# Kernel tuning notes

Hardware: AMD Instinct MI355X
Metric: run time of the kernel (lower is better)

The kernel has to match this reference:

```python
import jax, jax.numpy as jnp
import numpy as np


def _gru(x, w_ih, w_hh, b_ih, b_hh, reverse=False):
    # PyTorch GRU cell math. x: (N, T, Din) -> (N, T, Hh)
    N, T, _ = x.shape
    Hh = w_hh.shape[1]
    xp = jnp.einsum('ntd,gd->ntg', x, w_ih) + b_ih  # (N, T, 3*Hh), input gates precomputed

    def step(h, xp_t):
        gh = h @ w_hh.T + b_hh
        ir, iz, inn = jnp.split(xp_t, 3, axis=-1)
        hr, hz, hn = jnp.split(gh, 3, axis=-1)
        r = jax.nn.sigmoid(ir + hr)
        z = jax.nn.sigmoid(iz + hz)
        n = jnp.tanh(inn + r * hn)
        h_new = (1.0 - z) * n + z * h
        return h_new, h_new

    h0 = jnp.zeros((N, Hh), x.dtype)
    _, ys = jax.lax.scan(step, h0, jnp.swapaxes(xp, 0, 1), reverse=reverse)
    return jnp.swapaxes(ys, 0, 1)


def _bigru(x, pf, pb):
    return jnp.concatenate([_gru(x, *pf), _gru(x, *pb, reverse=True)], axis=-1)


def _attn(out, w, b, ctx):
    # out: (N, T, H). tanh(Linear) -> context dot -> softmax -> weighted sum
    u = jnp.tanh(jnp.einsum('nth,gh->ntg', out, w) + b)
    a = jax.nn.softmax(u @ ctx, axis=-1)  # (N, T)
    return jnp.einsum('nt,nth->nh', a, out)


def setup_inputs() -> dict:
    key = jax.random.key(0)
    H, Hh = 512, 256
    S, B, Nsent = 2048, 16, 16
    L = S // Nsent
    ks = jax.random.split(key, 32)

    def p(k, shape):
        return jax.random.normal(k, shape, jnp.float32) * 0.05

    starts = jnp.arange(Nsent, dtype=jnp.int32) * L
    spans = jnp.stack([starts, starts + L], axis=-1)  # (Nsent, 2)
    spans = jnp.broadcast_to(spans, (B, Nsent, 2))

    inp = {
        'token_feats': jax.random.normal(ks[0], (S, B, H), jnp.float32),
        'sentence_spans': spans,
        # word BiGRU params (forward / backward directions)
        'w_wih_f': p(ks[1], (3 * Hh, H)), 'w_whh_f': p(ks[2], (3 * Hh, Hh)),
        'w_bih_f': p(ks[3], (3 * Hh,)), 'w_bhh_f': p(ks[4], (3 * Hh,)),
        'w_wih_b': p(ks[5], (3 * Hh, H)), 'w_whh_b': p(ks[6], (3 * Hh, Hh)),
        'w_bih_b': p(ks[7], (3 * Hh,)), 'w_bhh_b': p(ks[8], (3 * Hh,)),
        # sentence BiGRU params
        's_wih_f': p(ks[9], (3 * Hh, H)), 's_whh_f': p(ks[10], (3 * Hh, Hh)),
        's_bih_f': p(ks[11], (3 * Hh,)), 's_bhh_f': p(ks[12], (3 * Hh,)),
        's_wih_b': p(ks[13], (3 * Hh, H)), 's_whh_b': p(ks[14], (3 * Hh, Hh)),
        's_bih_b': p(ks[15], (3 * Hh,)), 's_bhh_b': p(ks[16], (3 * Hh,)),
        # attention params
        'w_attn_w': p(ks[17], (H, H)), 'w_attn_b': p(ks[18], (H,)),
        'w_ctx': jax.random.normal(ks[19], (H,), jnp.float32),
        's_attn_w': p(ks[20], (H, H)), 's_attn_b': p(ks[21], (H,)),
        's_ctx': jax.random.normal(ks[22], (H,), jnp.float32),
    }
    return inp


def reference(token_feats, sentence_spans,
              w_wih_f, w_whh_f, w_bih_f, w_bhh_f,
              w_wih_b, w_whh_b, w_bih_b, w_bhh_b,
              s_wih_f, s_whh_f, s_bih_f, s_bhh_f,
              s_wih_b, s_whh_b, s_bih_b, s_bhh_b,
              w_attn_w, w_attn_b, w_ctx,
              s_attn_w, s_attn_b, s_ctx):
    S, B, H = token_feats.shape
    Nsent = sentence_spans.shape[1]
    L = S // Nsent  # uniform spans: segment b,i = tokens [i*L, (i+1)*L)

    x = jnp.swapaxes(token_feats, 0, 1)  # (B, S, H)
    segs = x.reshape(B * Nsent, L, H)    # all sentences batched together

    # word-level BiGRU + word attention -> sentence vectors
    out_w = _bigru(segs, (w_wih_f, w_whh_f, w_bih_f, w_bhh_f),
                   (w_wih_b, w_whh_b, w_bih_b, w_bhh_b))  # (B*Nsent, L, H)
    sent_vecs = _attn(out_w, w_attn_w, w_attn_b, w_ctx).reshape(B, Nsent, H)

    # sentence-level BiGRU + sentence attention (no padding: all masks true)
    out_s = _bigru(sent_vecs, (s_wih_f, s_whh_f, s_bih_f, s_bhh_f),
                   (s_wih_b, s_whh_b, s_bih_b, s_bhh_b))  # (B, Nsent, H)
    Yh = _attn(out_s, s_attn_w, s_attn_b, s_ctx)  # (B, H)
    return Yh
```

## Files before the change

kernel.cpp:

```cpp
#include <hip/hip_runtime.h>
#include <stdint.h>


using uint32  = unsigned int;
using bf16x8  = __attribute__((ext_vector_type(8))) __bf16;
using floatx4 = __attribute__((ext_vector_type(4))) float;

__device__ __forceinline__ float b2f(unsigned short u) {
    union { uint32 i; float f; } v; v.i = ((uint32)u) << 16; return v.f;
}
__device__ __forceinline__ unsigned short f2b(float f) {
    union { float f; uint32 i; } v; v.f = f;
    uint32 r = v.i + 0x7fffu + ((v.i >> 16) & 1u);
    return (unsigned short)(r >> 16);
}
__device__ __forceinline__ float sigmoidf_(float x) { return 1.f / (1.f + __expf(-x)); }
__device__ __forceinline__ float tanhf_(float x) {
    x = fminf(15.f, fmaxf(-15.f, x));
    float e = __expf(2.f * x);
    return (e - 1.f) / (e + 1.f);
}

__device__ __forceinline__ void gl16(const unsigned short* g, unsigned short* l) {
    __builtin_amdgcn_global_load_lds(
        (const __attribute__((address_space(1))) uint32*)g,
        (__attribute__((address_space(3))) uint32*)l, 16, 0, 0);
}

#define O_XPC     0L
#define O_OWHI    50331648L
#define O_OWLO    83886080L
#define O_STATE   117440512L
#define O_SCW     117964800L
#define O_W0HI    118095872L
#define O_W0LO    118882304L
#define O_W1HI    119668736L
#define O_W1LO    120455168L
#define O_WAHI    121241600L
#define O_WALO    121765888L
#define O_S0HI    122290176L
#define O_S0LO    123076608L
#define O_S1HI    123863040L
#define O_S1LO    124649472L
#define O_SAHI    125435904L
#define O_SALO    125960192L
#define O_HW0     126484480L
#define O_HW1     126877696L
#define O_HS0     127270912L
#define O_HS1     127664128L
#define O_SENTHI  128057344L
#define O_SENTLO  128319488L
#define O_XPS     128581632L
#define O_SSTATE  130154496L
#define O_OSHI    130187264L
#define O_OSLO    130449408L
#define O_SCS     130711552L
#define O_TKWH    130712576L
#define O_TKWL    164267008L

__global__ __launch_bounds__(256)
void cvt_hilo6(const float* __restrict__ s0, const float* __restrict__ s1,
               const float* __restrict__ s2, const float* __restrict__ s3,
               const float* __restrict__ s4, const float* __restrict__ s5,
               char* __restrict__ ws)
{
    const int b = blockIdx.x;
    const float* src; unsigned short *hi, *lo; int base;
    if (b < 192)      { src = s0; hi = (unsigned short*)(ws + O_W0HI); lo = (unsigned short*)(ws + O_W0LO); base = b; }
    else if (b < 384) { src = s1; hi = (unsigned short*)(ws + O_W1HI); lo = (unsigned short*)(ws + O_W1LO); base = b - 192; }
    else if (b < 576) { src = s2; hi = (unsigned short*)(ws + O_S0HI); lo = (unsigned short*)(ws + O_S0LO); base = b - 384; }
    else if (b < 768) { src = s3; hi = (unsigned short*)(ws + O_S1HI); lo = (unsigned short*)(ws + O_S1LO); base = b - 576; }
    else if (b < 896) { src = s4; hi = (unsigned short*)(ws + O_WAHI); lo = (unsigned short*)(ws + O_WALO); base = b - 768; }
    else              { src = s5; hi = (unsigned short*)(ws + O_SAHI); lo = (unsigned short*)(ws + O_SALO); base = b - 896; }
    const int idx = (base * 256 + threadIdx.x) * 8;
    float f[8];
    *reinterpret_cast<float4*>(&f[0]) = *reinterpret_cast<const float4*>(src + idx);
    *reinterpret_cast<float4*>(&f[4]) = *reinterpret_cast<const float4*>(src + idx + 4);
    unsigned short h[8], l[8];
    #pragma unroll
    for (int j = 0; j < 8; ++j) {
        h[j] = f2b(f[j]);
        l[j] = f2b(f[j] - b2f(h[j]));
    }
    *reinterpret_cast<uint4*>(hi + idx) = *reinterpret_cast<const uint4*>(h);
    *reinterpret_cast<uint4*>(lo + idx) = *reinterpret_cast<const uint4*>(l);
}

__global__ __launch_bounds__(256)
void cvt_b4(const float* __restrict__ s0, const float* __restrict__ s1,
            const float* __restrict__ s2, const float* __restrict__ s3,
            char* __restrict__ ws)
{
    const int b = blockIdx.x;
    const float* src; unsigned short* dst; int base;
    if (b < 96)       { src = s0; dst = (unsigned short*)(ws + O_HW0); base = b; }
    else if (b < 192) { src = s1; dst = (unsigned short*)(ws + O_HW1); base = b - 96; }
    else if (b < 288) { src = s2; dst = (unsigned short*)(ws + O_HS0); base = b - 192; }
    else              { src = s3; dst = (unsigned short*)(ws + O_HS1); base = b - 288; }
    const int idx = (base * 256 + threadIdx.x) * 8;
    float f[8];
    *reinterpret_cast<float4*>(&f[0]) = *reinterpret_cast<const float4*>(src + idx);
    *reinterpret_cast<float4*>(&f[4]) = *reinterpret_cast<const float4*>(src + idx + 4);
    unsigned short o[8];
    #pragma unroll
    for (int j = 0; j < 8; ++j) o[j] = f2b(f[j]);
    *reinterpret_cast<uint4*>(dst + idx) = *reinterpret_cast<const uint4*>(o);
}

__global__ __launch_bounds__(256)
void cvt_tokfull(const float* __restrict__ tok, unsigned short* __restrict__ whi,
                 unsigned short* __restrict__ wlo)
{
    const int u = blockIdx.x * 256 + threadIdx.x;
    const int h8 = u & 63;
    const int rest = u >> 6;
    const int t = rest & 127, seq = rest >> 7;
    const int sent = seq & 15, b = seq >> 4;
    const long src = ((long)(sent * 128 + t) * 16 + b) * 512 + h8 * 8;
    float f[8];
    *reinterpret_cast<float4*>(&f[0]) = *reinterpret_cast<const float4*>(tok + src);
    *reinterpret_cast<float4*>(&f[4]) = *reinterpret_cast<const float4*>(tok + src + 4);
    unsigned short h[8], l[8];
    #pragma unroll
    for (int j = 0; j < 8; ++j) {
        h[j] = f2b(f[j]);
        l[j] = f2b(f[j] - b2f(h[j]));
    }
    const long dst = (long)rest * 512 + h8 * 8;
    *reinterpret_cast<uint4*>(whi + dst) = *reinterpret_cast<const uint4*>(h);
    *reinterpret_cast<uint4*>(wlo + dst) = *reinterpret_cast<const uint4*>(l);
}

template<int AMODE>
__device__ __forceinline__ long amap(int m, int t0, int sgn) {
    if (AMODE == 1) {
        const int sq = m >> 5, tl = m & 31;
        return (long)(sq * 128 + t0 + sgn * tl) * 512;
    } else if (AMODE == 3) {
        const int n = m >> 4, tl = m & 15;
        return (long)(n * 16 + t0 + sgn * tl) * 512;
    }
    return (long)m * 512;
}

template<int AMODE, int OUT>
__global__ __launch_bounds__(256)
void gemm_p(const unsigned short* __restrict__ Ahi, const unsigned short* __restrict__ Alo,
            const unsigned short* __restrict__ Wh0, const unsigned short* __restrict__ Wl0,
            const unsigned short* __restrict__ Wh1, const unsigned short* __restrict__ Wl1,
            const float* __restrict__ b0, const float* __restrict__ b1,
            float* __restrict__ C, int ldC, long c1off,
            float* __restrict__ score, const float* __restrict__ ctx,
            int t00, int t01, int nbyHalf)
{
    __shared__ __align__(16) unsigned short smem[3 * 8192];

    int bx = blockIdx.x, by = blockIdx.y;
    {
        const int nbx = gridDim.x, nby = gridDim.y;
        if ((nby & 7) == 0) {
            const int l = by * nbx + bx;
            const int xcd = l & 7;
            const int s = l >> 3;
            bx = s % nbx;
            by = xcd * (nby >> 3) + s / nbx;
        }
    }

    const int tid  = threadIdx.x;
    const int lane = tid & 63;
    const int wave = tid >> 6;
    const int wm = wave >> 1, wn = wave & 1;
    const int n_base = bx * 128;
    const int q = lane >> 4;
    const int r = lane & 15;

    const unsigned short* Whi = Wh0;
    const unsigned short* Wlo = Wl0;
    const float* bias = b0;
    float* Cb = C;
    int t0 = t00, sgn = 1, m_base;
    if (nbyHalf > 0 && by >= nbyHalf) {
        Whi = Wh1; Wlo = Wl1; bias = b1; Cb = C + c1off;
        t0 = t01; sgn = -1;
        m_base = (by - nbyHalf) * 128;
    } else {
        m_base = by * 128;
    }

    long aoff[2], woff[2];
    #pragma unroll
    for (int i = 0; i < 2; ++i) {
        const int s = tid + 256 * i;
        const int R = s >> 2, kg = s & 3;
        const int kq = (kg - (R >> 1)) & 3;
        aoff[i] = amap<AMODE>(m_base + R, t0, sgn) + kq * 8;
        woff[i] = (long)(n_base + R) * 512 + kq * 8;
    }

    floatx4 acc[4][4];
    #pragma unroll
    for (int mt = 0; mt < 4; ++mt)
        #pragma unroll
        for (int nt = 0; nt < 4; ++nt) acc[mt][nt] = (floatx4){0.f, 0.f, 0.f, 0.f};

    auto stage = [&](int ts) {
        const int buf = ts % 3;
        const int kr  = ts >> 4;
        const int kk  = (ts & 15) * 32;
        const unsigned short* Ap = (kr == 2) ? Alo : Ahi;
        const unsigned short* Wp = (kr == 1) ? Wlo : Whi;
        unsigned short* LA = smem + buf * 8192;
        unsigned short* LW = LA + 4096;
        #pragma unroll
        for (int i = 0; i < 2; ++i) {
            gl16(Ap + aoff[i] + kk, LA + (tid + 256 * i) * 8);
            gl16(Wp + woff[i] + kk, LW + (tid + 256 * i) * 8);
        }
    };

    stage(0);
    stage(1);
    for (int t = 0; t < 48; ++t) {
        stage(t + 2 < 48 ? t + 2 : 47);
        asm volatile("s_waitcnt vmcnt(8)\n\ts_barrier" ::: "memory");

        const unsigned short* LA = smem + (t % 3) * 8192;
        const unsigned short* LW = LA + 4096;
        bf16x8 ah[4], wh[4];
        #pragma unroll
        for (int mt = 0; mt < 4; ++mt) {
            const int R = wm * 64 + mt * 16 + r;
            ah[mt] = *reinterpret_cast<const bf16x8*>(LA + (R * 4 + ((q + (R >> 1)) & 3)) * 8);
        }
        #pragma unroll
        for (int nt = 0; nt < 4; ++nt) {
            const int Rn = wn * 64 + nt * 16 + r;
            wh[nt] = *reinterpret_cast<const bf16x8*>(LW + (Rn * 4 + ((q + (Rn >> 1)) & 3)) * 8);
        }
        #pragma unroll
        for (int nt = 0; nt < 4; ++nt)
            #pragma unroll
            for (int mt = 0; mt < 4; ++mt)
                acc[mt][nt] = __builtin_amdgcn_mfma_f32_16x16x32_bf16(ah[mt], wh[nt], acc[mt][nt], 0, 0, 0);

        asm volatile("s_waitcnt lgkmcnt(0)\n\ts_barrier" ::: "memory");
    }
    asm volatile("s_waitcnt vmcnt(0)" ::: "memory");

    if (OUT == 0) {
        #pragma unroll
        for (int nt = 0; nt < 4; ++nt) {
            const int n = n_base + wn * 64 + nt * 16 + r;
            const float bs = bias[n];
            #pragma unroll
            for (int mt = 0; mt < 4; ++mt) {
                const int m = m_base + wm * 64 + mt * 16 + q * 4;
                #pragma unroll
                for (int e = 0; e < 4; ++e)
                    Cb[(long)(m + e) * ldC + n] = acc[mt][nt][e] + bs;
            }
        }
    } else {
        #pragma unroll
        for (int mt = 0; mt < 4; ++mt) {
            float p[4] = {0.f, 0.f, 0.f, 0.f};
            #pragma unroll
            for (int nt = 0; nt < 4; ++nt) {
                const int n = n_base + wn * 64 + nt * 16 + r;
                const float cx = ctx[n];
                const float bs = bias[n];
                #pragma unroll
                for (int e = 0; e < 4; ++e)
                    p[e] += cx * tanhf_(acc[mt][nt][e] + bs);
            }
            #pragma unroll
            for (int mk = 1; mk < 16; mk <<= 1) {
                #pragma unroll
                for (int e = 0; e < 4; ++e) p[e] += __shfl_xor(p[e], mk, 64);
            }
            if (r == 0) {
                const int m = m_base + wm * 64 + mt * 16 + q * 4;
                #pragma unroll
                for (int e = 0; e < 4; ++e)
                    atomicAdd(&score[m + e], p[e]);
            }
        }
    }
}

__global__ __launch_bounds__(512, 2)
void gru2(const float* __restrict__ xp,
          const unsigned short* __restrict__ Wf,
          const unsigned short* __restrict__ Wb,
          const float* __restrict__ bhf, const float* __restrict__ bhb,
          float* __restrict__ state,
          unsigned short* __restrict__ ohi, unsigned short* __restrict__ olo,
          int steps, int t0f, int t0b, int groups, int Tout)
{
    __shared__ float pre[768 * 5];
    __shared__ unsigned short Bf[8 * 64 * 8];

    const int tid  = threadIdx.x;
    const int lane = tid & 63;
    const int w    = tid >> 6;
    const int dir  = blockIdx.x / groups;
    const int g    = blockIdx.x % groups;
    const int nseq = groups * 2;
    const unsigned short* W = dir ? Wb : Wf;
    const float* bh = dir ? bhb : bhf;
    const int t0  = dir ? t0b : t0f;
    const int sgn = dir ? -1 : 1;

    const int s = tid >> 8;
    const int j = tid & 255;
    const float bhr = bh[j], bhz = bh[j + 256], bhn = bh[j + 512];

    bf16x8 wf[6][8];
    {
        const int r0 = w * 96 + (lane & 15);
        const int kf = (lane >> 4) * 8;
        #pragma unroll
        for (int mt = 0; mt < 6; ++mt)
            #pragma unroll
            for (int kk = 0; kk < 8; ++kk)
                wf[mt][kk] = *reinterpret_cast<const bf16x8*>(
                    W + (long)(r0 + mt * 16) * 256 + kk * 32 + kf);
    }

    #pragma unroll
    for (int i = 0; i < 4; ++i)
        reinterpret_cast<uint32*>(Bf)[tid * 4 + i] = 0;

    float h = state[((long)dir * nseq + g * 2 + s) * 256 + j];
    const int posHi = ((j >> 5) * 64 + ((j >> 3) & 3) * 16 + s) * 8 + (j & 7);
    const int posLo = ((j >> 5) * 64 + ((j >> 3) & 3) * 16 + 2 + s) * 8 + (j & 7);
    {
        const unsigned short hb = f2b(h);
        Bf[posHi] = hb;
        Bf[posLo] = f2b(h - b2f(hb));
    }
    asm volatile("s_waitcnt lgkmcnt(0)\n\ts_barrier" ::: "memory");

    const float* xbase = xp + (long)dir * nseq * steps * 768
                       + (long)(g * 2 + s) * steps * 768;
    const int q = lane >> 4, r = lane & 15;

    float xr = xbase[j], xz = xbase[256 + j], xn = xbase[512 + j];

    for (int st = 0; st < steps; ++st) {
        const int t = t0 + sgn * st;

        const int sn = (st + 1 < steps) ? st + 1 : st;
        const float* xb = xbase + (long)sn * 768;
        const float nxr = xb[j];
        const float nxz = xb[256 + j];
        const float nxn = xb[512 + j];

        floatx4 acc[6];
        #pragma unroll
        for (int mt = 0; mt < 6; ++mt) acc[mt] = (floatx4){0.f, 0.f, 0.f, 0.f};
        #pragma unroll
        for (int kk = 0; kk < 8; ++kk) {
            bf16x8 bv = *reinterpret_cast<const bf16x8*>(Bf + (kk * 64 + lane) * 8);
            #pragma unroll
            for (int mt = 0; mt < 6; ++mt)
                acc[mt] = __builtin_amdgcn_mfma_f32_16x16x32_bf16(wf[mt][kk], bv, acc[mt], 0, 0, 0);
        }
        if (r < 4) {
            #pragma unroll
            for (int mt = 0; mt < 6; ++mt) {
                const int row = w * 96 + mt * 16 + q * 4;
                #pragma unroll
                for (int e = 0; e < 4; ++e)
                    pre[(row + e) * 5 + r] = acc[mt][e];
            }
        }
        asm volatile("s_waitcnt lgkmcnt(0)\n\ts_barrier" ::: "memory");

        {
            const float pr = pre[j * 5 + s]         + pre[j * 5 + 2 + s];
            const float pz = pre[(j + 256) * 5 + s] + pre[(j + 256) * 5 + 2 + s];
            const float pn = pre[(j + 512) * 5 + s] + pre[(j + 512) * 5 + 2 + s];
            const float rg = sigmoidf_(xr + pr + bhr);
            const float zg = sigmoidf_(xz + pz + bhz);
            const float nn = tanhf_(xn + rg * (pn + bhn));
            h = (1.f - zg) * nn + zg * h;
            const unsigned short hb = f2b(h);
            const unsigned short lb = f2b(h - b2f(hb));
            Bf[posHi] = hb;
            Bf[posLo] = lb;
            const long orow = ((long)(g * 2 + s) * Tout + t) * 512 + dir * 256 + j;
            ohi[orow] = hb;
            olo[orow] = lb;
        }
        xr = nxr; xz = nxz; xn = nxn;
        asm volatile("s_waitcnt lgkmcnt(0)\n\ts_barrier" ::: "memory");
    }

    state[((long)dir * nseq + g * 2 + s) * 256 + j] = h;
}

template<int MODE, int T>
__global__ __launch_bounds__(256)
void attn_wsum(const float* __restrict__ score,
               const unsigned short* __restrict__ fhi,
               const unsigned short* __restrict__ flo,
               void* __restrict__ o1, void* __restrict__ o2)
{
    const int n = blockIdx.x;
    const int tid = threadIdx.x;
    __shared__ float a[T];
    __shared__ float e[T];
    if (tid < T) a[tid] = score[n * T + tid];
    __syncthreads();
    float mx = -1e30f;
    #pragma unroll
    for (int t = 0; t < T; ++t) mx = fmaxf(mx, a[t]);
    if (tid < T) e[tid] = __expf(a[tid] - mx);
    __syncthreads();
    float sm = 0.f;
    #pragma unroll
    for (int t = 0; t < T; ++t) sm += e[t];
    const float inv = 1.f / sm;
    float acc0 = 0.f, acc1 = 0.f;
    #pragma unroll 8
    for (int t = 0; t < T; ++t) {
        const float w = e[t] * inv;
        const long base = ((long)n * T + t) * 512;
        acc0 += w * (b2f(fhi[base + tid])       + b2f(flo[base + tid]));
        acc1 += w * (b2f(fhi[base + tid + 256]) + b2f(flo[base + tid + 256]));
    }
    if (MODE == 1) {
        float* o = (float*)o1;
        o[n * 512 + tid] = acc0;
        o[n * 512 + tid + 256] = acc1;
    } else {
        unsigned short* oh = (unsigned short*)o1;
        unsigned short* ol = (unsigned short*)o2;
        const unsigned short h0 = f2b(acc0), h1 = f2b(acc1);
        oh[n * 512 + tid]       = h0;  ol[n * 512 + tid]       = f2b(acc0 - b2f(h0));
        oh[n * 512 + tid + 256] = h1;  ol[n * 512 + tid + 256] = f2b(acc1 - b2f(h1));
    }
}

extern "C" void kernel_launch(void* const* d_in, const int* in_sizes, int n_in,
                              void* d_out, int out_size, void* d_ws, size_t ws_size,
                              hipStream_t stream) {
    const float* tok      = (const float*)d_in[0];
    const float* w_wih_f  = (const float*)d_in[2];
    const float* w_whh_f  = (const float*)d_in[3];
    const float* w_bih_f  = (const float*)d_in[4];
    const float* w_bhh_f  = (const float*)d_in[5];
    const float* w_wih_b  = (const float*)d_in[6];
    const float* w_whh_b  = (const float*)d_in[7];
    const float* w_bih_b  = (const float*)d_in[8];
    const float* w_bhh_b  = (const float*)d_in[9];
    const float* s_wih_f  = (const float*)d_in[10];
    const float* s_whh_f  = (const float*)d_in[11];
    const float* s_bih_f  = (const float*)d_in[12];
    const float* s_bhh_f  = (const float*)d_in[13];
    const float* s_wih_b  = (const float*)d_in[14];
    const float* s_whh_b  = (const float*)d_in[15];
    const float* s_bih_b  = (const float*)d_in[16];
    const float* s_bhh_b  = (const float*)d_in[17];
    const float* w_attn_b = (const float*)d_in[19];
    const float* w_ctx    = (const float*)d_in[20];
    const float* s_attn_b = (const float*)d_in[22];
    const float* s_ctx    = (const float*)d_in[23];

    char* ws = (char*)d_ws;
    float*          xpc   = (float*)(ws + O_XPC);
    unsigned short* owhi  = (unsigned short*)(ws + O_OWHI);
    unsigned short* owlo  = (unsigned short*)(ws + O_OWLO);
    float*          state = (float*)(ws + O_STATE);
    float*          score_w = (float*)(ws + O_SCW);
    unsigned short* W0HI  = (unsigned short*)(ws + O_W0HI);
    unsigned short* W0LO  = (unsigned short*)(ws + O_W0LO);
    unsigned short* W1HI  = (unsigned short*)(ws + O_W1HI);
    unsigned short* W1LO  = (unsigned short*)(ws + O_W1LO);
    unsigned short* WAHI  = (unsigned short*)(ws + O_WAHI);
    unsigned short* WALO  = (unsigned short*)(ws + O_WALO);
    unsigned short* S0HI  = (unsigned short*)(ws + O_S0HI);
    unsigned short* S0LO  = (unsigned short*)(ws + O_S0LO);
    unsigned short* S1HI  = (unsigned short*)(ws + O_S1HI);
    unsigned short* S1LO  = (unsigned short*)(ws + O_S1LO);
    unsigned short* SAHI  = (unsigned short*)(ws + O_SAHI);
    unsigned short* SALO  = (unsigned short*)(ws + O_SALO);
    unsigned short* HW0   = (unsigned short*)(ws + O_HW0);
    unsigned short* HW1   = (unsigned short*)(ws + O_HW1);
    unsigned short* HS0   = (unsigned short*)(ws + O_HS0);
    unsigned short* HS1   = (unsigned short*)(ws + O_HS1);
    unsigned short* senthi = (unsigned short*)(ws + O_SENTHI);
    unsigned short* sentlo = (unsigned short*)(ws + O_SENTLO);
    float*          xp_s  = (float*)(ws + O_XPS);
    float*          sstate = (float*)(ws + O_SSTATE);
    unsigned short* oshi  = (unsigned short*)(ws + O_OSHI);
    unsigned short* oslo  = (unsigned short*)(ws + O_OSLO);
    float*          score_s = (float*)(ws + O_SCS);
    unsigned short* tkwh  = (unsigned short*)(ws + O_TKWH);
    unsigned short* tkwl  = (unsigned short*)(ws + O_TKWL);

    const dim3 blk(256);

    hipMemsetAsync(ws + O_STATE,  0, 524288, stream);
    hipMemsetAsync(ws + O_SSTATE, 0, 32768, stream);
    hipMemsetAsync(ws + O_SCW,    0, 131072, stream);
    hipMemsetAsync(ws + O_SCS,    0, 1024, stream);

    cvt_hilo6<<<dim3(1024), blk, 0, stream>>>(w_wih_f, w_wih_b, s_wih_f, s_wih_b,
                                              (const float*)d_in[18], (const float*)d_in[21], ws);
    cvt_b4<<<dim3(384), blk, 0, stream>>>(w_whh_f, w_whh_b, s_whh_f, s_whh_b, ws);
    cvt_tokfull<<<dim3(8192), blk, 0, stream>>>(tok, tkwh, tkwl);

    const long XDW = 256L * 32 * 768;
    for (int c = 0; c < 4; ++c) {
        gemm_p<1, 0><<<dim3(6, 128), blk, 0, stream>>>(
            tkwh, tkwl, W0HI, W0LO, W1HI, W1LO, w_bih_f, w_bih_b,
            xpc, 768, XDW, nullptr, nullptr, 32 * c, 127 - 32 * c, 64);
        gru2<<<dim3(256), dim3(512), 0, stream>>>(
            xpc, HW0, HW1, w_bhh_f, w_bhh_b, state, owhi, owlo,
            32, 32 * c, 127 - 32 * c, 128, 128);
    }

    gemm_p<2, 1><<<dim3(4, 256), blk, 0, stream>>>(
        owhi, owlo, WAHI, WALO, WAHI, WALO, w_attn_b, w_attn_b,
        nullptr, 0, 0, score_w, w_ctx, 0, 0, 0);
    attn_wsum<0, 128><<<dim3(256), blk, 0, stream>>>(score_w, owhi, owlo, senthi, sentlo);

    const long XDS = 16L * 16 * 768;
    gemm_p<3, 0><<<dim3(6, 4), blk, 0, stream>>>(
        senthi, sentlo, S0HI, S0LO, S1HI, S1LO, s_bih_f, s_bih_b,
        xp_s, 768, XDS, nullptr, nullptr, 0, 15, 2);

    gru2<<<dim3(16), dim3(512), 0, stream>>>(
        xp_s, HS0, HS1, s_bhh_f, s_bhh_b, sstate, oshi, oslo,
        16, 0, 15, 8, 16);

    gemm_p<2, 1><<<dim3(4, 2), blk, 0, stream>>>(
        oshi, oslo, SAHI, SALO, SAHI, SALO, s_attn_b, s_attn_b,
        nullptr, 0, 0, score_s, s_ctx, 0, 0, 0);
    attn_wsum<1, 16><<<dim3(16), blk, 0, stream>>>(score_s, oshi, oslo, d_out, nullptr);
}
```

Measured before the change: 724.0 us.

## Load hi/lo operand tiles together and issue three split-bf16 MFMAs per k-step

The split-precision GEMM used to walk K three times (hi*hi, hi*lo, lo*hi), reloading the A and W tiles on every pass across 48 triple-buffered stages. It now loads Ahi, Alo, Whi and Wlo for one K slice into a double buffer and issues all three MFMA products from those registers. That cuts the number of global-to-LDS tile loads and the number of barrier rounds to 16 stages. In exchange, LDS per block grows to 64KB and the prefetch depth drops from two stages to one, which could lower occupancy or expose more load latency.

```diff
diff --git a/kernel.cpp b/kernel.cpp
--- a/kernel.cpp
+++ b/kernel.cpp
@@ -145,7 +145,7 @@
 
 template<int AMODE, int OUT>
 __global__ __launch_bounds__(256)
-void gemm_p(const unsigned short* __restrict__ Ahi, const unsigned short* __restrict__ Alo,
+void gemm_d(const unsigned short* __restrict__ Ahi, const unsigned short* __restrict__ Alo,
             const unsigned short* __restrict__ Wh0, const unsigned short* __restrict__ Wl0,
             const unsigned short* __restrict__ Wh1, const unsigned short* __restrict__ Wl1,
             const float* __restrict__ b0, const float* __restrict__ b1,
@@ -153,7 +153,7 @@
             float* __restrict__ score, const float* __restrict__ ctx,
             int t00, int t01, int nbyHalf)
 {
-    __shared__ __align__(16) unsigned short smem[3 * 8192];
+    __shared__ __align__(16) unsigned short smem[2 * 16384];
 
     int bx = blockIdx.x, by = blockIdx.y;
     {
@@ -205,45 +205,45 @@
         for (int nt = 0; nt < 4; ++nt) acc[mt][nt] = (floatx4){0.f, 0.f, 0.f, 0.f};
 
     auto stage = [&](int ts) {
-        const int buf = ts % 3;
-        const int kr  = ts >> 4;
-        const int kk  = (ts & 15) * 32;
-        const unsigned short* Ap = (kr == 2) ? Alo : Ahi;
-        const unsigned short* Wp = (kr == 1) ? Wlo : Whi;
-        unsigned short* LA = smem + buf * 8192;
-        unsigned short* LW = LA + 4096;
+        const int k0 = ts * 32;
+        unsigned short* B = smem + (ts & 1) * 16384;
         #pragma unroll
         for (int i = 0; i < 2; ++i) {
-            gl16(Ap + aoff[i] + kk, LA + (tid + 256 * i) * 8);
-            gl16(Wp + woff[i] + kk, LW + (tid + 256 * i) * 8);
+            const int ld = (tid + 256 * i) * 8;
+            gl16(Ahi + aoff[i] + k0, B + ld);
+            gl16(Alo + aoff[i] + k0, B + 4096 + ld);
+            gl16(Whi + woff[i] + k0, B + 8192 + ld);
+            gl16(Wlo + woff[i] + k0, B + 12288 + ld);
         }
     };
 
     stage(0);
-    stage(1);
-    for (int t = 0; t < 48; ++t) {
-        stage(t + 2 < 48 ? t + 2 : 47);
+    for (int t = 0; t < 16; ++t) {
+        stage(t + 1 < 16 ? t + 1 : 15);
         asm volatile("s_waitcnt vmcnt(8)\n\ts_barrier" ::: "memory");
 
-        const unsigned short* LA = smem + (t % 3) * 8192;
-        const unsigned short* LW = LA + 4096;
-        bf16x8 ah[4], wh[4];
+        const unsigned short* B = smem + (t & 1) * 16384;
+        bf16x8 ah[4], al[4];
         #pragma unroll
         for (int mt = 0; mt < 4; ++mt) {
             const int R = wm * 64 + mt * 16 + r;
-            ah[mt] = *reinterpret_cast<const bf16x8*>(LA + (R * 4 + ((q + (R >> 1)) & 3)) * 8);
+            const int s = R * 4 + ((q + (R >> 1)) & 3);
+            ah[mt] = *reinterpret_cast<const bf16x8*>(B + s * 8);
+            al[mt] = *reinterpret_cast<const bf16x8*>(B + 4096 + s * 8);
         }
         #pragma unroll
         for (int nt = 0; nt < 4; ++nt) {
             const int Rn = wn * 64 + nt * 16 + r;
-            wh[nt] = *reinterpret_cast<const bf16x8*>(LW + (Rn * 4 + ((q + (Rn >> 1)) & 3)) * 8);
-        }
-        #pragma unroll
-        for (int nt = 0; nt < 4; ++nt)
-            #pragma unroll
-            for (int mt = 0; mt < 4; ++mt)
-                acc[mt][nt] = __builtin_amdgcn_mfma_f32_16x16x32_bf16(ah[mt], wh[nt], acc[mt][nt], 0, 0, 0);
-
+            const int sn = Rn * 4 + ((q + (Rn >> 1)) & 3);
+            bf16x8 wh = *reinterpret_cast<const bf16x8*>(B + 8192 + sn * 8);
+            bf16x8 wl = *reinterpret_cast<const bf16x8*>(B + 12288 + sn * 8);
+            #pragma unroll
+            for (int mt = 0; mt < 4; ++mt) {
+                acc[mt][nt] = __builtin_amdgcn_mfma_f32_16x16x32_bf16(ah[mt], wh, acc[mt][nt], 0, 0, 0);
+                acc[mt][nt] = __builtin_amdgcn_mfma_f32_16x16x32_bf16(ah[mt], wl, acc[mt][nt], 0, 0, 0);
+                acc[mt][nt] = __builtin_amdgcn_mfma_f32_16x16x32_bf16(al[mt], wh, acc[mt][nt], 0, 0, 0);
+            }
+        }
         asm volatile("s_waitcnt lgkmcnt(0)\n\ts_barrier" ::: "memory");
     }
     asm volatile("s_waitcnt vmcnt(0)" ::: "memory");
@@ -515,7 +515,7 @@
 
     const long XDW = 256L * 32 * 768;
     for (int c = 0; c < 4; ++c) {
-        gemm_p<1, 0><<<dim3(6, 128), blk, 0, stream>>>(
+        gemm_d<1, 0><<<dim3(6, 128), blk, 0, stream>>>(
             tkwh, tkwl, W0HI, W0LO, W1HI, W1LO, w_bih_f, w_bih_b,
             xpc, 768, XDW, nullptr, nullptr, 32 * c, 127 - 32 * c, 64);
         gru2<<<dim3(256), dim3(512), 0, stream>>>(
@@ -523,13 +523,13 @@
             32, 32 * c, 127 - 32 * c, 128, 128);
     }
 
-    gemm_p<2, 1><<<dim3(4, 256), blk, 0, stream>>>(
+    gemm_d<2, 1><<<dim3(4, 256), blk, 0, stream>>>(
         owhi, owlo, WAHI, WALO, WAHI, WALO, w_attn_b, w_attn_b,
         nullptr, 0, 0, score_w, w_ctx, 0, 0, 0);
     attn_wsum<0, 128><<<dim3(256), blk, 0, stream>>>(score_w, owhi, owlo, senthi, sentlo);
 
     const long XDS = 16L * 16 * 768;
-    gemm_p<3, 0><<<dim3(6, 4), blk, 0, stream>>>(
+    gemm_d<3, 0><<<dim3(6, 4), blk, 0, stream>>>(
         senthi, sentlo, S0HI, S0LO, S1HI, S1LO, s_bih_f, s_bih_b,
         xp_s, 768, XDS, nullptr, nullptr, 0, 15, 2);
 
@@ -537,7 +537,7 @@
         xp_s, HS0, HS1, s_bhh_f, s_bhh_b, sstate, oshi, oslo,
         16, 0, 15, 8, 16);
 
-    gemm_p<2, 1><<<dim3(4, 2), blk, 0, stream>>>(
+    gemm_d<2, 1><<<dim3(4, 2), blk, 0, stream>>>(
         oshi, oslo, SAHI, SALO, SAHI, SALO, s_attn_b, s_attn_b,
         nullptr, 0, 0, score_s, s_ctx, 0, 0, 0);
     attn_wsum<1, 16><<<dim3(16), blk, 0, stream>>>(score_s, oshi, oslo, d_out, nullptr);
```

Result: faster. 687.7 us (-5.0%).
